# Performance work log

Measured on AMD Instinct MI355X. Metric: run time of the kernel, lower is better.

## Reference

```python
import jax, jax.numpy as jnp
import numpy as np

ALPHA = 0.2  # LeakyReLU negative slope
NEG_FILL = -9e15


def setup_inputs() -> dict:
    key = jax.random.key(0)
    k_adj, k_x, k_W, k_a = jax.random.split(key, 4)
    n, in_feats, out_feats = 12288, 256, 64
    adj = jax.random.randint(k_adj, (n, n), 0, 2, dtype=jnp.int32)
    x = jax.random.normal(k_x, (n, in_feats), dtype=jnp.float32)
    W = jax.random.normal(k_W, (in_feats, out_feats), dtype=jnp.float32) * 0.1
    a = jax.random.normal(k_a, (2 * out_feats, 1), dtype=jnp.float32) * 0.1
    return {"adj": adj, "x": x, "W": W, "a": a}


def reference(adj, x, W, a):
    out_feats = W.shape[1]
    h = x @ W                                  # (n, out_feats)
    wh1 = h @ a[:out_feats]                    # (n, 1)
    wh2 = h @ a[out_feats:]                    # (n, 1)
    e = jax.nn.leaky_relu(wh1 + wh2, ALPHA)    # (n, 1) -- faithful to source (no transpose)
    # broadcast (n,1) scores against (n,n) adjacency mask
    attention = jnp.where(adj > 0, e, NEG_FILL)
    attention = jax.nn.softmax(attention, axis=1)
    # dropout p=0.0 -> identity (eval mode)
    h_prime = attention @ h                    # (n, out_feats)
    return jax.nn.elu(h_prime)                 # concat=True
```

## Files before the change

### kernel.cpp

```cpp
#include <hip/hip_runtime.h>

#define N_NODES 12288
#define IN_F    256
#define OUT_F   64
#define KSPLIT  4
#define MT      64
#define KC      (N_NODES / KSPLIT)
#define STEPS   (KC / 32)

typedef __attribute__((ext_vector_type(8))) short bf16x8;
typedef __attribute__((ext_vector_type(4))) float f32x4;

__device__ __forceinline__ unsigned short f2bf(float f) {
    union { float f; unsigned int i; } v; v.f = f;
    unsigned int x = v.i;
    unsigned int r = x + 0x7FFFu + ((x >> 16) & 1u);
    return (unsigned short)(r >> 16);
}

__global__ __launch_bounds__(256) void k_hT(const float* __restrict__ x,
                                            const float* __restrict__ W,
                                            unsigned short* __restrict__ hT) {
    __shared__ unsigned short WT[OUT_F][IN_F + 8];
    int tid = threadIdx.x;
    for (int idx = tid; idx < IN_F * OUT_F; idx += 256) {
        int k = idx >> 6, n = idx & 63;
        WT[n][k] = f2bf(W[idx]);
    }
    __syncthreads();

    int lane = tid & 63, wave = tid >> 6;
    int q = lane >> 4, ml = lane & 15;
    int i0 = blockIdx.x * MT;
    int row = i0 + 16 * wave + ml;
    const float* xr = x + (size_t)row * IN_F + 8 * q;

    f32x4 acc[4];
    #pragma unroll
    for (int nt = 0; nt < 4; ++nt) acc[nt] = (f32x4){0.f, 0.f, 0.f, 0.f};

    #pragma unroll
    for (int kk = 0; kk < IN_F; kk += 32) {
        float4 x0 = *(const float4*)(xr + kk);
        float4 x1 = *(const float4*)(xr + kk + 4);
        union { bf16x8 v; unsigned short u[8]; } A;
        A.u[0] = f2bf(x0.x); A.u[1] = f2bf(x0.y); A.u[2] = f2bf(x0.z); A.u[3] = f2bf(x0.w);
        A.u[4] = f2bf(x1.x); A.u[5] = f2bf(x1.y); A.u[6] = f2bf(x1.z); A.u[7] = f2bf(x1.w);
        #pragma unroll
        for (int nt = 0; nt < 4; ++nt) {
            bf16x8 bv = *(const bf16x8*)&WT[16 * nt + ml][kk + 8 * q];
            acc[nt] = __builtin_amdgcn_mfma_f32_16x16x32_bf16(A.v, bv, acc[nt], 0, 0, 0);
        }
    }

    #pragma unroll
    for (int nt = 0; nt < 4; ++nt) {
        ushort4 o;
        o.x = f2bf(acc[nt][0]); o.y = f2bf(acc[nt][1]);
        o.z = f2bf(acc[nt][2]); o.w = f2bf(acc[nt][3]);
        *(ushort4*)&hT[(size_t)(16 * nt + ml) * N_NODES + i0 + 16 * wave + 4 * q] = o;
    }
}

__global__ __launch_bounds__(256) void k_spmm(const int* __restrict__ adj,
                                              const unsigned short* __restrict__ hT,
                                              float* __restrict__ s_part,
                                              int* __restrict__ deg_part) {
    const int tid  = threadIdx.x;
    const int lane = tid & 63;
    const int wave = tid >> 6;
    const int q    = lane >> 4;
    const int ml   = lane & 15;
    const int i0   = blockIdx.x * MT;
    const int ks   = blockIdx.y;
    const int k0   = ks * KC;
    const int row  = i0 + 16 * wave + ml;

    const int* ap = adj + (size_t)row * N_NODES + k0 + 8 * q;
    const unsigned short* bp = hT + (size_t)ml * N_NODES + k0 + 8 * q;

    f32x4 acc[4];
    #pragma unroll
    for (int nt = 0; nt < 4; ++nt) acc[nt] = (f32x4){0.f, 0.f, 0.f, 0.f};
    unsigned int degp = 0;

#define LOADS(s, A0, A1, B0, B1, B2, B3) do {                                  \
    A0 = *(const int4*)(ap + 32 * (s));                                        \
    A1 = *(const int4*)(ap + 32 * (s) + 4);                                    \
    B0 = *(const uint4*)(bp + 32 * (s));                                       \
    B1 = *(const uint4*)(bp + (size_t)16 * N_NODES + 32 * (s));                \
    B2 = *(const uint4*)(bp + (size_t)32 * N_NODES + 32 * (s));                \
    B3 = *(const uint4*)(bp + (size_t)48 * N_NODES + 32 * (s));                \
} while (0)

#define COMP(A0, A1, B0, B1, B2, B3) do {                                      \
    unsigned int t0 = (unsigned int)A0.x + ((unsigned int)A0.y << 16);         \
    unsigned int t1 = (unsigned int)A0.z + ((unsigned int)A0.w << 16);         \
    unsigned int t2 = (unsigned int)A1.x + ((unsigned int)A1.y << 16);         \
    unsigned int t3 = (unsigned int)A1.z + ((unsigned int)A1.w << 16);         \
    degp += t0 + t1 + t2 + t3;                                                 \
    union { bf16x8 v; unsigned int w[4]; } av_;                                \
    av_.w[0] = t0 * 0x3F80u; av_.w[1] = t1 * 0x3F80u;                          \
    av_.w[2] = t2 * 0x3F80u; av_.w[3] = t3 * 0x3F80u;                          \
    acc[0] = __builtin_amdgcn_mfma_f32_16x16x32_bf16(av_.v, *(const bf16x8*)&B0, acc[0], 0, 0, 0); \
    acc[1] = __builtin_amdgcn_mfma_f32_16x16x32_bf16(av_.v, *(const bf16x8*)&B1, acc[1], 0, 0, 0); \
    acc[2] = __builtin_amdgcn_mfma_f32_16x16x32_bf16(av_.v, *(const bf16x8*)&B2, acc[2], 0, 0, 0); \
    acc[3] = __builtin_amdgcn_mfma_f32_16x16x32_bf16(av_.v, *(const bf16x8*)&B3, acc[3], 0, 0, 0); \
} while (0)

    int4 a0A, a1A; uint4 b0A, b1A, b2A, b3A;
    int4 a0B, a1B; uint4 b0B, b1B, b2B, b3B;

    LOADS(0, a0A, a1A, b0A, b1A, b2A, b3A);
    for (int s = 0; s < STEPS - 2; s += 2) {
        LOADS(s + 1, a0B, a1B, b0B, b1B, b2B, b3B);
        COMP(a0A, a1A, b0A, b1A, b2A, b3A);
        LOADS(s + 2, a0A, a1A, b0A, b1A, b2A, b3A);
        COMP(a0B, a1B, b0B, b1B, b2B, b3B);
    }
    LOADS(STEPS - 1, a0B, a1B, b0B, b1B, b2B, b3B);
    COMP(a0A, a1A, b0A, b1A, b2A, b3A);
    COMP(a0B, a1B, b0B, b1B, b2B, b3B);

#undef LOADS
#undef COMP

    float* sp = s_part + (size_t)ks * ((size_t)N_NODES * OUT_F);
    #pragma unroll
    for (int nt = 0; nt < 4; ++nt) {
        #pragma unroll
        for (int rr = 0; rr < 4; ++rr) {
            int orow = i0 + 16 * wave + 4 * q + rr;
            int ocol = 16 * nt + ml;
            sp[(size_t)orow * OUT_F + ocol] = acc[nt][rr];
        }
    }

    degp += (unsigned int)__shfl_xor((int)degp, 16, 64);
    degp += (unsigned int)__shfl_xor((int)degp, 32, 64);
    int deg = (int)((degp & 0xFFFFu) + (degp >> 16));
    if (q == 0)
        deg_part[ks * N_NODES + row] = deg;
}

__global__ __launch_bounds__(256) void k_out(const float* __restrict__ s_part,
                                             const int* __restrict__ deg_part,
                                             float* __restrict__ out) {
    int idx = blockIdx.x * 256 + threadIdx.x;
    int i = idx >> 6;
    float s = 0.f; int deg = 0;
    #pragma unroll
    for (int p = 0; p < KSPLIT; ++p) {
        s   += s_part[(size_t)p * ((size_t)N_NODES * OUT_F) + idx];
        deg += deg_part[p * N_NODES + i];
    }
    float v = (deg > 0) ? (s / (float)deg) : 0.f;
    out[idx] = (v > 0.f) ? v : expm1f(v);
}

extern "C" void kernel_launch(void* const* d_in, const int* in_sizes, int n_in,
                              void* d_out, int out_size, void* d_ws, size_t ws_size,
                              hipStream_t stream) {
    const int*   adj = (const int*)d_in[0];
    const float* x   = (const float*)d_in[1];
    const float* W   = (const float*)d_in[2];
    float* out = (float*)d_out;

    char* ws = (char*)d_ws;
    const size_t hT_bytes = (size_t)N_NODES * OUT_F * 2;
    const size_t sp_bytes = (size_t)KSPLIT * N_NODES * OUT_F * 4;
    unsigned short* hT = (unsigned short*)ws;
    float* s_part      = (float*)(ws + hT_bytes);
    int*   deg_part    = (int*)(ws + hT_bytes + sp_bytes);

    k_hT  <<<dim3(N_NODES / MT),          dim3(256), 0, stream>>>(x, W, hT);
    k_spmm<<<dim3(N_NODES / MT, KSPLIT),  dim3(256), 0, stream>>>(adj, hT, s_part, deg_part);
    k_out <<<dim3(N_NODES * OUT_F / 256), dim3(256), 0, stream>>>(s_part, deg_part, out);
}
```

Before: 896.1 us.

## Stage adjacency tiles through LDS with coalesced row loads and MFMA degree count

The SpMM kernel now loads adjacency in wide, contiguous per-row chunks: each lane reads an int2, 16 rows per wave, in 128-column steps. It packs the chunks to bf16 0/1 values in a wave-private, double-buffered LDS tile, and the MFMA A fragments are read back from that tile. The neighbour count is now an extra MFMA against a ones vector instead of packed integer adds and shuffles, and it is stored as float. The aim is better global-load coalescing and more bytes in flight on the dominant adjacency stream. The cost is extra LDS traffic, register pressure from 16 staged int2 loads, and one more MFMA per step.

```diff
diff --git a/kernel.cpp b/kernel.cpp
--- a/kernel.cpp
+++ b/kernel.cpp
@@ -6,7 +6,9 @@
 #define KSPLIT  4
 #define MT      64
 #define KC      (N_NODES / KSPLIT)
-#define STEPS   (KC / 32)
+#define BK      128
+#define STEPS   (KC / BK)
+#define AST     144
 
 typedef __attribute__((ext_vector_type(8))) short bf16x8;
 typedef __attribute__((ext_vector_type(4))) float f32x4;
@@ -65,7 +67,9 @@
 __global__ __launch_bounds__(256) void k_spmm(const int* __restrict__ adj,
                                               const unsigned short* __restrict__ hT,
                                               float* __restrict__ s_part,
-                                              int* __restrict__ deg_part) {
+                                              float* __restrict__ deg_part) {
+    __shared__ __align__(16) unsigned short As[2][4][16][AST];
+
     const int tid  = threadIdx.x;
     const int lane = tid & 63;
     const int wave = tid >> 6;
@@ -74,55 +78,82 @@
     const int i0   = blockIdx.x * MT;
     const int ks   = blockIdx.y;
     const int k0   = ks * KC;
-    const int row  = i0 + 16 * wave + ml;
-
-    const int* ap = adj + (size_t)row * N_NODES + k0 + 8 * q;
+
+    const int* arow = adj + (size_t)(i0 + 16 * wave) * N_NODES + k0 + 2 * lane;
     const unsigned short* bp = hT + (size_t)ml * N_NODES + k0 + 8 * q;
 
-    f32x4 acc[4];
+    union { bf16x8 v; unsigned short u[8]; } ones;
+    #pragma unroll
+    for (int i = 0; i < 8; ++i) ones.u[i] = 0x3F80;
+
+    f32x4 acc[4], accd;
     #pragma unroll
     for (int nt = 0; nt < 4; ++nt) acc[nt] = (f32x4){0.f, 0.f, 0.f, 0.f};
-    unsigned int degp = 0;
-
-#define LOADS(s, A0, A1, B0, B1, B2, B3) do {                                  \
-    A0 = *(const int4*)(ap + 32 * (s));                                        \
-    A1 = *(const int4*)(ap + 32 * (s) + 4);                                    \
-    B0 = *(const uint4*)(bp + 32 * (s));                                       \
-    B1 = *(const uint4*)(bp + (size_t)16 * N_NODES + 32 * (s));                \
-    B2 = *(const uint4*)(bp + (size_t)32 * N_NODES + 32 * (s));                \
-    B3 = *(const uint4*)(bp + (size_t)48 * N_NODES + 32 * (s));                \
-} while (0)
-
-#define COMP(A0, A1, B0, B1, B2, B3) do {                                      \
-    unsigned int t0 = (unsigned int)A0.x + ((unsigned int)A0.y << 16);         \
-    unsigned int t1 = (unsigned int)A0.z + ((unsigned int)A0.w << 16);         \
-    unsigned int t2 = (unsigned int)A1.x + ((unsigned int)A1.y << 16);         \
-    unsigned int t3 = (unsigned int)A1.z + ((unsigned int)A1.w << 16);         \
-    degp += t0 + t1 + t2 + t3;                                                 \
-    union { bf16x8 v; unsigned int w[4]; } av_;                                \
-    av_.w[0] = t0 * 0x3F80u; av_.w[1] = t1 * 0x3F80u;                          \
-    av_.w[2] = t2 * 0x3F80u; av_.w[3] = t3 * 0x3F80u;                          \
-    acc[0] = __builtin_amdgcn_mfma_f32_16x16x32_bf16(av_.v, *(const bf16x8*)&B0, acc[0], 0, 0, 0); \
-    acc[1] = __builtin_amdgcn_mfma_f32_16x16x32_bf16(av_.v, *(const bf16x8*)&B1, acc[1], 0, 0, 0); \
-    acc[2] = __builtin_amdgcn_mfma_f32_16x16x32_bf16(av_.v, *(const bf16x8*)&B2, acc[2], 0, 0, 0); \
-    acc[3] = __builtin_amdgcn_mfma_f32_16x16x32_bf16(av_.v, *(const bf16x8*)&B3, acc[3], 0, 0, 0); \
-} while (0)
-
-    int4 a0A, a1A; uint4 b0A, b1A, b2A, b3A;
-    int4 a0B, a1B; uint4 b0B, b1B, b2B, b3B;
-
-    LOADS(0, a0A, a1A, b0A, b1A, b2A, b3A);
-    for (int s = 0; s < STEPS - 2; s += 2) {
-        LOADS(s + 1, a0B, a1B, b0B, b1B, b2B, b3B);
-        COMP(a0A, a1A, b0A, b1A, b2A, b3A);
-        LOADS(s + 2, a0A, a1A, b0A, b1A, b2A, b3A);
-        COMP(a0B, a1B, b0B, b1B, b2B, b3B);
-    }
-    LOADS(STEPS - 1, a0B, a1B, b0B, b1B, b2B, b3B);
-    COMP(a0A, a1A, b0A, b1A, b2A, b3A);
-    COMP(a0B, a1B, b0B, b1B, b2B, b3B);
-
-#undef LOADS
+    accd = (f32x4){0.f, 0.f, 0.f, 0.f};
+
+    int2 st[16];
+
+#define STAGE_ISSUE(sidx) do {                                                 \
+    const int* ap_ = arow + (size_t)(sidx) * BK;                               \
+    _Pragma("unroll")                                                          \
+    for (int rr = 0; rr < 16; ++rr)                                            \
+        st[rr] = *(const int2*)(ap_ + (size_t)rr * N_NODES);                   \
+} while (0)
+
+#define STAGE_WRITE(b) do {                                                    \
+    _Pragma("unroll")                                                          \
+    for (int rr = 0; rr < 16; ++rr) {                                          \
+        unsigned int t = ((unsigned int)st[rr].x +                             \
+                          ((unsigned int)st[rr].y << 16)) * 0x3F80u;           \
+        *(unsigned int*)&As[b][wave][rr][2 * lane] = t;                        \
+    }                                                                          \
+} while (0)
+
+#define BLOAD(koff, B0, B1, B2, B3) do {                                       \
+    const unsigned short* bq = bp + (koff);                                    \
+    B0 = *(const uint4*)(bq);                                                  \
+    B1 = *(const uint4*)(bq + (size_t)16 * N_NODES);                           \
+    B2 = *(const uint4*)(bq + (size_t)32 * N_NODES);                           \
+    B3 = *(const uint4*)(bq + (size_t)48 * N_NODES);                           \
+} while (0)
+
+#define COMP(j, b, B0, B1, B2, B3) do {                                        \
+    bf16x8 av = *(const bf16x8*)&As[b][wave][ml][32 * (j) + 8 * q];            \
+    acc[0] = __builtin_amdgcn_mfma_f32_16x16x32_bf16(av, *(const bf16x8*)&B0, acc[0], 0, 0, 0); \
+    acc[1] = __builtin_amdgcn_mfma_f32_16x16x32_bf16(av, *(const bf16x8*)&B1, acc[1], 0, 0, 0); \
+    acc[2] = __builtin_amdgcn_mfma_f32_16x16x32_bf16(av, *(const bf16x8*)&B2, acc[2], 0, 0, 0); \
+    acc[3] = __builtin_amdgcn_mfma_f32_16x16x32_bf16(av, *(const bf16x8*)&B3, acc[3], 0, 0, 0); \
+    accd   = __builtin_amdgcn_mfma_f32_16x16x32_bf16(av, ones.v,               accd,   0, 0, 0); \
+} while (0)
+
+    uint4 b0A, b1A, b2A, b3A;
+    uint4 b0B, b1B, b2B, b3B;
+
+    STAGE_ISSUE(0);
+    STAGE_WRITE(0);
+    BLOAD(0, b0A, b1A, b2A, b3A);
+
+    for (int s = 0; s < STEPS; ++s) {
+        const int b  = s & 1;
+        const int s1 = (s + 1 < STEPS) ? s + 1 : 0;
+
+        STAGE_ISSUE(s1);
+
+        BLOAD(BK * s + 32, b0B, b1B, b2B, b3B);
+        COMP(0, b, b0A, b1A, b2A, b3A);
+        BLOAD(BK * s + 64, b0A, b1A, b2A, b3A);
+        COMP(1, b, b0B, b1B, b2B, b3B);
+        BLOAD(BK * s + 96, b0B, b1B, b2B, b3B);
+        COMP(2, b, b0A, b1A, b2A, b3A);
+        BLOAD(BK * s1,     b0A, b1A, b2A, b3A);
+        COMP(3, b, b0B, b1B, b2B, b3B);
+
+        STAGE_WRITE(b ^ 1);
+    }
+
+#undef STAGE_ISSUE
+#undef STAGE_WRITE
+#undef BLOAD
 #undef COMP
 
     float* sp = s_part + (size_t)ks * ((size_t)N_NODES * OUT_F);
@@ -136,25 +167,25 @@
         }
     }
 
-    degp += (unsigned int)__shfl_xor((int)degp, 16, 64);
-    degp += (unsigned int)__shfl_xor((int)degp, 32, 64);
-    int deg = (int)((degp & 0xFFFFu) + (degp >> 16));
-    if (q == 0)
-        deg_part[ks * N_NODES + row] = deg;
+    if (ml == 0) {
+        #pragma unroll
+        for (int rr = 0; rr < 4; ++rr)
+            deg_part[ks * N_NODES + i0 + 16 * wave + 4 * q + rr] = accd[rr];
+    }
 }
 
 __global__ __launch_bounds__(256) void k_out(const float* __restrict__ s_part,
-                                             const int* __restrict__ deg_part,
+                                             const float* __restrict__ deg_part,
                                              float* __restrict__ out) {
     int idx = blockIdx.x * 256 + threadIdx.x;
     int i = idx >> 6;
-    float s = 0.f; int deg = 0;
+    float s = 0.f, deg = 0.f;
     #pragma unroll
     for (int p = 0; p < KSPLIT; ++p) {
         s   += s_part[(size_t)p * ((size_t)N_NODES * OUT_F) + idx];
         deg += deg_part[p * N_NODES + i];
     }
-    float v = (deg > 0) ? (s / (float)deg) : 0.f;
+    float v = (deg > 0.5f) ? (s / deg) : 0.f;
     out[idx] = (v > 0.f) ? v : expm1f(v);
 }
 
@@ -171,7 +202,7 @@
     const size_t sp_bytes = (size_t)KSPLIT * N_NODES * OUT_F * 4;
     unsigned short* hT = (unsigned short*)ws;
     float* s_part      = (float*)(ws + hT_bytes);
-    int*   deg_part    = (int*)(ws + hT_bytes + sp_bytes);
+    float* deg_part    = (float*)(ws + hT_bytes + sp_bytes);
 
     k_hT  <<<dim3(N_NODES / MT),          dim3(256), 0, stream>>>(x, W, hT);
     k_spmm<<<dim3(N_NODES / MT, KSPLIT),  dim3(256), 0, stream>>>(adj, hT, s_part, deg_part);
```

Result: faster. 851.9 us (-4.9%).
